# Performance work log

Hardware: AMD Instinct MI355X
Metric: run time of the kernel (lower is better)

The kernel has to match this reference:

```python
import jax, jax.numpy as jnp
import numpy as np

UNITS = 256


def setup_inputs() -> dict:
    key = jax.random.key(0)
    ks = jax.random.split(key, 9)
    B, H, W, C = 8, 64, 64, UNITS
    x = jax.random.normal(ks[0], (B, H, W, C), dtype=jnp.float32)
    # 1x1 Conv2D == per-pixel linear: weight [C_in, C_out], bias [C_out]
    def lin(k):
        return jax.random.normal(k, (C, UNITS), dtype=jnp.float32) * (2.0 / C) ** 0.5
    return {
        "x": x,
        "wq": lin(ks[1]), "bq": jnp.zeros((UNITS,), jnp.float32),
        "wk": lin(ks[2]), "bk": jnp.zeros((UNITS,), jnp.float32),
        "wv": lin(ks[3]), "bv": jnp.zeros((UNITS,), jnp.float32),
        "wp": lin(ks[4]), "bp": jnp.zeros((UNITS,), jnp.float32),
    }


def reference(x, wq, bq, wk, bk, wv, bv, wp, bp):
    B, H, W, C = x.shape
    N = H * W
    scale = jnp.asarray(UNITS, jnp.float32) ** -0.5
    xf = x.reshape(B, N, C)  # 1x1 conv == matmul over channels
    q = xf @ wq + bq
    k = xf @ wk + bk
    v = xf @ wv + bv
    # (b,h,w,c)x(b,H,W,c)->(b,h,w,H,W) flattened to (b,N,N)
    scores = jnp.einsum('bnc,bmc->bnm', q, k) * scale
    attn = jax.nn.softmax(scores, axis=-1)
    out = jnp.einsum('bnm,bmc->bnc', attn, v)
    proj = out @ wp + bp
    return x + proj.reshape(B, H, W, UNITS)
```

## Files before the change

kernel.cpp:

```cpp
#include <hip/hip_runtime.h>


typedef _Float16 half8 __attribute__((ext_vector_type(8)));
typedef _Float16 half4 __attribute__((ext_vector_type(4)));
typedef float f32x4 __attribute__((ext_vector_type(4)));
typedef float f32x16 __attribute__((ext_vector_type(16)));
typedef unsigned int u32x4 __attribute__((ext_vector_type(4)));
typedef unsigned int u32x2 __attribute__((ext_vector_type(2)));

#define MFMA16(a, b, c) __builtin_amdgcn_mfma_f32_16x16x32_f16((a), (b), (c), 0, 0, 0)
#define MFMA32(a, b, c) __builtin_amdgcn_mfma_f32_32x32x16_f16((a), (b), (c), 0, 0, 0)

#if __has_builtin(__builtin_amdgcn_exp2f)
#define EXP2(x) __builtin_amdgcn_exp2f(x)
#else
#define EXP2(x) exp2f(x)
#endif

#define QSCALE 0.09016843898f
#define ESHIFT 11.5415603f

__device__ __forceinline__ void lds_load16(const void* g, void* l) {
    __builtin_amdgcn_global_load_lds(
        (const __attribute__((address_space(1))) unsigned int*)g,
        (__attribute__((address_space(3))) unsigned int*)l, 16, 0, 0);
}

__global__ __launch_bounds__(256)
void wt_prep(const float* __restrict__ w0, const float* __restrict__ w1,
             const float* __restrict__ w2, const float* __restrict__ w3,
             _Float16* __restrict__ outw)
{
    __shared__ _Float16 sT[64 * 72];
    const int z = blockIdx.z;
    const float* W = (z == 0) ? w0 : (z == 1) ? w1 : (z == 2) ? w2 : w3;
    _Float16* O = outw + z * 65536;
    const int kb = blockIdx.x * 64, nb = blockIdx.y * 64;
    const int t = threadIdx.x;
    const int r = t >> 4, c4 = (t & 15) * 4;
#pragma unroll
    for (int i = 0; i < 4; ++i) {
        f32x4 ld = *(const f32x4*)(W + (size_t)(kb + r + i * 16) * 256 + nb + c4);
#pragma unroll
        for (int j = 0; j < 4; ++j) sT[(c4 + j) * 72 + r + i * 16] = (_Float16)ld[j];
    }
    __syncthreads();
#pragma unroll
    for (int i = 0; i < 4; ++i) {
        int n = r + i * 16;
        *(u32x2*)&O[(size_t)(nb + n) * 256 + kb + c4] = *(const u32x2*)&sT[n * 72 + c4];
    }
}

__global__ __launch_bounds__(256)
void qkv_gemm(const float* __restrict__ x, const _Float16* __restrict__ wt,
              const float* __restrict__ bq, const float* __restrict__ bk,
              const float* __restrict__ bv,
              _Float16* __restrict__ qo, _Float16* __restrict__ ko,
              _Float16* __restrict__ vo)
{
    __shared__ _Float16 smem[4 * 2560];
    _Float16* sA = smem;

    const int tid  = threadIdx.x;
    const int w    = tid >> 6;
    const int lane = tid & 63;
    const int quad = lane >> 4;
    const int l16  = lane & 15;
    const int m0   = blockIdx.x * 64;
    const int n0   = blockIdx.y * 64;
    const int rS = tid >> 2, cS = (tid & 3) << 3;

    const float* ap = x + (size_t)(m0 + rS) * 256 + cS;
    f32x4 a0 = *(const f32x4*)ap, a1 = *(const f32x4*)(ap + 4);
    u32x4 bst[3];
#pragma unroll
    for (int o = 0; o < 3; ++o)
        bst[o] = *(const u32x4*)(wt + o * 65536 + (size_t)(n0 + rS) * 256 + cS);

    f32x4 zero4 = {0.f, 0.f, 0.f, 0.f};
    f32x4 acc[3][4];
#pragma unroll
    for (int o = 0; o < 3; ++o)
#pragma unroll
        for (int mt = 0; mt < 4; ++mt) acc[o][mt] = zero4;

    for (int it = 0; it < 8; ++it) {
        __syncthreads();
        half8 t;
#pragma unroll
        for (int j = 0; j < 4; ++j) { t[j] = (_Float16)a0[j]; t[j + 4] = (_Float16)a1[j]; }
        *(half8*)&sA[rS * 40 + cS] = t;
#pragma unroll
        for (int o = 0; o < 3; ++o)
            *(u32x4*)&smem[2560 * (o + 1) + rS * 40 + cS] = bst[o];
        __syncthreads();
        if (it < 7) {
            int k0 = (it + 1) * 32;
            const float* ap2 = x + (size_t)(m0 + rS) * 256 + k0 + cS;
            a0 = *(const f32x4*)ap2; a1 = *(const f32x4*)(ap2 + 4);
#pragma unroll
            for (int o = 0; o < 3; ++o)
                bst[o] = *(const u32x4*)(wt + o * 65536 + (size_t)(n0 + rS) * 256 + k0 + cS);
        }
        half8 af[4];
#pragma unroll
        for (int mt = 0; mt < 4; ++mt)
            af[mt] = *(const half8*)&sA[(mt * 16 + l16) * 40 + quad * 8];
#pragma unroll
        for (int o = 0; o < 3; ++o) {
            half8 bf = *(const half8*)&smem[2560 * (o + 1) + (16 * w + l16) * 40 + quad * 8];
#pragma unroll
            for (int mt = 0; mt < 4; ++mt)
                acc[o][mt] = MFMA16(af[mt], bf, acc[o][mt]);
        }
    }

    const int col = n0 + 16 * w + l16;
#pragma unroll
    for (int mt = 0; mt < 4; ++mt) {
#pragma unroll
        for (int reg = 0; reg < 4; ++reg) {
            int row = m0 + 16 * mt + quad * 4 + reg;
            qo[(size_t)row * 256 + col] = (_Float16)((acc[0][mt][reg] + bq[col]) * QSCALE);
            ko[(size_t)row * 256 + col] = (_Float16)(acc[1][mt][reg] + bk[col]);
        }
    }
    __syncthreads();
    _Float16* sT = smem;
#pragma unroll
    for (int mt = 0; mt < 4; ++mt)
#pragma unroll
        for (int reg = 0; reg < 4; ++reg)
            sT[(16 * w + l16) * 72 + 16 * mt + quad * 4 + reg] =
                (_Float16)(acc[2][mt][reg] + bv[col]);
    __syncthreads();
    int ch = tid >> 2, po = (tid & 3) << 4;
    int bb = m0 >> 12, pix = m0 & 4095;
    _Float16* dst = vo + (size_t)bb * 1048576 + (size_t)(n0 + ch) * 4096 + pix + po;
    *(u32x4*)dst       = *(const u32x4*)&sT[ch * 72 + po];
    *(u32x4*)(dst + 8) = *(const u32x4*)&sT[ch * 72 + po + 8];
}

__global__ __launch_bounds__(256)
void proj_gemm(const _Float16* __restrict__ opart, const float* __restrict__ lpart,
               const _Float16* __restrict__ Wt, const float* __restrict__ bias,
               const float* __restrict__ resid, float* __restrict__ out)
{
    __shared__ _Float16 smem[2 * 2560];
    _Float16* sA = smem;
    _Float16* sB = smem + 2560;

    const int tid  = threadIdx.x;
    const int w    = tid >> 6;
    const int lane = tid & 63;
    const int quad = lane >> 4;
    const int l16  = lane & 15;
    const int m0   = blockIdx.x * 64;
    const int n0   = blockIdx.y * 64;
    const int rS = tid >> 2, cS = (tid & 3) << 3;

    const _Float16* o1p = opart;
    const _Float16* o2p = opart + 8388608;
    const int row = m0 + rS;
    const float inv = 1.0f / (lpart[row] + lpart[32768 + row]);

    u32x4 a1v = *(const u32x4*)(o1p + (size_t)row * 256 + cS);
    u32x4 a2v = *(const u32x4*)(o2p + (size_t)row * 256 + cS);
    u32x4 bst = *(const u32x4*)(Wt + (size_t)(n0 + rS) * 256 + cS);

    f32x4 zero4 = {0.f, 0.f, 0.f, 0.f};
    f32x4 acc[4] = {zero4, zero4, zero4, zero4};

    for (int it = 0; it < 8; ++it) {
        __syncthreads();
        {
            half8 h1 = *(half8*)&a1v, h2 = *(half8*)&a2v, t;
#pragma unroll
            for (int j = 0; j < 8; ++j)
                t[j] = (_Float16)(((float)h1[j] + (float)h2[j]) * inv);
            *(half8*)&sA[rS * 40 + cS] = t;
        }
        *(u32x4*)&sB[rS * 40 + cS] = bst;
        __syncthreads();
        if (it < 7) {
            int k0 = (it + 1) * 32;
            a1v = *(const u32x4*)(o1p + (size_t)row * 256 + k0 + cS);
            a2v = *(const u32x4*)(o2p + (size_t)row * 256 + k0 + cS);
            bst = *(const u32x4*)(Wt + (size_t)(n0 + rS) * 256 + k0 + cS);
        }
        half8 af = *(const half8*)&sA[(16 * w + l16) * 40 + quad * 8];
#pragma unroll
        for (int nt = 0; nt < 4; ++nt) {
            half8 bf = *(const half8*)&sB[(nt * 16 + l16) * 40 + quad * 8];
            acc[nt] = MFMA16(af, bf, acc[nt]);
        }
    }
#pragma unroll
    for (int nt = 0; nt < 4; ++nt) {
#pragma unroll
        for (int reg = 0; reg < 4; ++reg) {
            int orow = m0 + 16 * w + quad * 4 + reg;
            int col = n0 + nt * 16 + l16;
            out[(size_t)orow * 256 + col] =
                acc[nt][reg] + bias[col] + resid[(size_t)orow * 256 + col];
        }
    }
}

__global__ __launch_bounds__(512, 2)
void attn_kernel(const _Float16* __restrict__ q, const _Float16* __restrict__ k,
                 const _Float16* __restrict__ vt, _Float16* __restrict__ opart,
                 float* __restrict__ lpart)
{
    extern __shared__ char smem[];
    char* sKb = smem;
    char* sVb = smem + 32768;

    const int tid  = threadIdx.x;
    const int w    = tid >> 6;
    const int lane = tid & 63;
    const int l31  = lane & 31;
    const int hi   = lane >> 5;
    const int kh   = blockIdx.x & 1;
    const int qg   = (blockIdx.x >> 1) & 15;
    const int b    = blockIdx.x >> 5;

    const _Float16* kb = k  + (size_t)b * 1048576 + (size_t)kh * 524288;
    const _Float16* vb = vt + (size_t)b * 1048576 + kh * 2048;
    const int rowbase = qg * 256 + w * 32;

    half8 qf[16];
    {
        const _Float16* q0 = q + (size_t)(b * 4096 + rowbase + l31) * 256 + hi * 8;
#pragma unroll
        for (int s = 0; s < 16; ++s) qf[s] = *(const half8*)(q0 + s * 16);
    }

    f32x16 o[8];
#pragma unroll
    for (int i = 0; i < 8; ++i)
#pragma unroll
        for (int j = 0; j < 16; ++j) o[i][j] = 0.f;
    float ls = 0.f;

    const int koffL = l31 * 256 + hi * 8;

#pragma unroll
    for (int j = 0; j < 2; ++j) {
        int s = w * 2 + j;
        lds_load16(kb + koffL + s * 16, sKb + s * 1024);
        int ct = s >> 1, ks = s & 1;
        lds_load16(vb + (size_t)(32 * ct + l31) * 4096 + 16 * ks + 8 * hi,
                   sVb + s * 1024);
    }

    for (int kt = 0; kt < 64; ++kt) {
        const int p = kt & 1;
        __syncthreads();

        if (kt < 63) {
            const _Float16* ktb = kb + (size_t)(kt + 1) * 8192;
            const _Float16* vtb = vb + (kt + 1) * 32;
            char* dK = sKb + (1 - p) * 16384;
            char* dV = sVb + (1 - p) * 16384;
#pragma unroll
            for (int j = 0; j < 2; ++j) {
                int s = w * 2 + j;
                lds_load16(ktb + koffL + s * 16, dK + s * 1024);
                int ct = s >> 1, ks = s & 1;
                lds_load16(vtb + (size_t)(32 * ct + l31) * 4096 + 16 * ks + 8 * hi,
                           dV + s * 1024);
            }
        }

        const char* K = sKb + p * 16384;
        const char* V = sVb + p * 16384;

        f32x16 saA, saB;
#pragma unroll
        for (int j = 0; j < 16; ++j) { saA[j] = 0.f; saB[j] = 0.f; }
#pragma unroll
        for (int s = 0; s < 16; s += 2) {
            half8 a0 = *(const half8*)(K + s * 1024 + lane * 16);
            half8 a1 = *(const half8*)(K + (s + 1) * 1024 + lane * 16);
            saA = MFMA32(a0, qf[s], saA);
            saB = MFMA32(a1, qf[s + 1], saB);
        }

#pragma unroll
        for (int j = 0; j < 16; ++j) saA[j] += saB[j];
        unsigned int c[8];
#pragma unroll
        for (int qq = 0; qq < 4; ++qq) {
            float p0 = EXP2(saA[qq * 4 + 0] - ESHIFT);
            float p1 = EXP2(saA[qq * 4 + 1] - ESHIFT);
            float p2 = EXP2(saA[qq * 4 + 2] - ESHIFT);
            float p3 = EXP2(saA[qq * 4 + 3] - ESHIFT);
            ls += (p0 + p1) + (p2 + p3);
            c[2 * qq]     = __builtin_bit_cast(unsigned int,
                                __builtin_amdgcn_cvt_pkrtz(p0, p1));
            c[2 * qq + 1] = __builtin_bit_cast(unsigned int,
                                __builtin_amdgcn_cvt_pkrtz(p2, p3));
        }
        u32x2 s0 = __builtin_amdgcn_permlane32_swap(c[0], c[2], false, false);
        u32x2 s1 = __builtin_amdgcn_permlane32_swap(c[1], c[3], false, false);
        u32x2 s2 = __builtin_amdgcn_permlane32_swap(c[4], c[6], false, false);
        u32x2 s3 = __builtin_amdgcn_permlane32_swap(c[5], c[7], false, false);
        u32x4 w0 = {s0[0], s1[0], s0[1], s1[1]};
        u32x4 w1 = {s2[0], s3[0], s2[1], s3[1]};
        half8 pf0 = __builtin_bit_cast(half8, w0);
        half8 pf1 = __builtin_bit_cast(half8, w1);

#pragma unroll
        for (int ct = 0; ct < 8; ++ct) {
            half8 b0 = *(const half8*)(V + (ct * 2 + 0) * 1024 + lane * 16);
            half8 b1 = *(const half8*)(V + (ct * 2 + 1) * 1024 + lane * 16);
            o[ct] = MFMA32(pf0, b0, o[ct]);
            o[ct] = MFMA32(pf1, b1, o[ct]);
        }
    }

    ls += __shfl_xor(ls, 32);
    _Float16* po = opart + (size_t)kh * 8388608 + (size_t)(b * 4096 + rowbase) * 256;
    float* pl = lpart + kh * 32768 + b * 4096 + rowbase;
    if (hi == 0) pl[l31] = ls;
#pragma unroll
    for (int ct = 0; ct < 8; ++ct) {
#pragma unroll
        for (int reg = 0; reg < 16; ++reg) {
            int row = (reg & 3) + 8 * (reg >> 2) + 4 * hi;
            po[(size_t)row * 256 + ct * 32 + l31] = (_Float16)o[ct][reg];
        }
    }
}

extern "C" void kernel_launch(void* const* d_in, const int* in_sizes, int n_in,
                              void* d_out, int out_size, void* d_ws, size_t ws_size,
                              hipStream_t stream) {
    const float* x  = (const float*)d_in[0];
    const float* wq = (const float*)d_in[1];
    const float* bq = (const float*)d_in[2];
    const float* wk = (const float*)d_in[3];
    const float* bk = (const float*)d_in[4];
    const float* wv = (const float*)d_in[5];
    const float* bv = (const float*)d_in[6];
    const float* wp = (const float*)d_in[7];
    const float* bp = (const float*)d_in[8];

    _Float16* qws  = (_Float16*)d_ws;
    _Float16* kws  = qws + 8388608;
    _Float16* vtws = kws + 8388608;
    _Float16* ows  = vtws + 8388608;
    _Float16* wt   = ows + 16777216;
    float*    lws  = (float*)(wt + 262144);

    dim3 blk(256);

    (void)hipFuncSetAttribute((const void*)attn_kernel,
                              hipFuncAttributeMaxDynamicSharedMemorySize, 65536);

    wt_prep<<<dim3(4, 4, 4), blk, 0, stream>>>(wq, wk, wv, wp, wt);
    qkv_gemm<<<dim3(512, 4), blk, 0, stream>>>(x, wt, bq, bk, bv, qws, kws, vtws);
    attn_kernel<<<dim3(256), dim3(512), 65536, stream>>>(qws, kws, vtws, ows, lws);
    proj_gemm<<<dim3(512, 4), blk, 0, stream>>>(ows, lws, wt + 196608, bp, x, (float*)d_out);
}
```

Before: 291.2 us.

## Stage full-K A tile in LDS once and stream B fragments from registers

```diff
diff --git a/kernel.cpp b/kernel.cpp
--- a/kernel.cpp
+++ b/kernel.cpp
@@ -52,15 +52,14 @@
     }
 }
 
-__global__ __launch_bounds__(256)
+__global__ __launch_bounds__(256, 4)
 void qkv_gemm(const float* __restrict__ x, const _Float16* __restrict__ wt,
               const float* __restrict__ bq, const float* __restrict__ bk,
               const float* __restrict__ bv,
               _Float16* __restrict__ qo, _Float16* __restrict__ ko,
               _Float16* __restrict__ vo)
 {
-    __shared__ _Float16 smem[4 * 2560];
-    _Float16* sA = smem;
+    __shared__ _Float16 sA[16384];
 
     const int tid  = threadIdx.x;
     const int w    = tid >> 6;
@@ -69,14 +68,27 @@
     const int l16  = lane & 15;
     const int m0   = blockIdx.x * 64;
     const int n0   = blockIdx.y * 64;
-    const int rS = tid >> 2, cS = (tid & 3) << 3;
-
-    const float* ap = x + (size_t)(m0 + rS) * 256 + cS;
-    f32x4 a0 = *(const f32x4*)ap, a1 = *(const f32x4*)(ap + 4);
-    u32x4 bst[3];
+    const int rS = tid >> 2, jS = tid & 3;
+
+    {
+        const float* ap = x + (size_t)(m0 + rS) * 256 + jS * 8;
+        const int blk_base = (rS >> 4) * 64 + jS * 16 + (rS & 15);
+#pragma unroll
+        for (int i = 0; i < 8; ++i) {
+            f32x4 a0 = *(const f32x4*)(ap + 32 * i);
+            f32x4 a1 = *(const f32x4*)(ap + 32 * i + 4);
+            half8 t;
+#pragma unroll
+            for (int j = 0; j < 4; ++j) { t[j] = (_Float16)a0[j]; t[j + 4] = (_Float16)a1[j]; }
+            *(half8*)&sA[(i * 256 + blk_base) * 8] = t;
+        }
+    }
+
+    const int nrow = (n0 + 16 * w + l16) * 256 + quad * 8;
+    u32x4 bcur[3];
 #pragma unroll
     for (int o = 0; o < 3; ++o)
-        bst[o] = *(const u32x4*)(wt + o * 65536 + (size_t)(n0 + rS) * 256 + cS);
+        bcur[o] = *(const u32x4*)(wt + o * 65536 + nrow);
 
     f32x4 zero4 = {0.f, 0.f, 0.f, 0.f};
     f32x4 acc[3][4];
@@ -85,35 +97,27 @@
 #pragma unroll
         for (int mt = 0; mt < 4; ++mt) acc[o][mt] = zero4;
 
+    __syncthreads();
+
     for (int it = 0; it < 8; ++it) {
-        __syncthreads();
-        half8 t;
-#pragma unroll
-        for (int j = 0; j < 4; ++j) { t[j] = (_Float16)a0[j]; t[j + 4] = (_Float16)a1[j]; }
-        *(half8*)&sA[rS * 40 + cS] = t;
+        half8 af[4];
+#pragma unroll
+        for (int mt = 0; mt < 4; ++mt)
+            af[mt] = *(const half8*)&sA[((it * 4 + mt) * 64 + quad * 16 + l16) * 8];
+        u32x4 bnext[3];
+        int itn = (it + 1) & 7;
 #pragma unroll
         for (int o = 0; o < 3; ++o)
-            *(u32x4*)&smem[2560 * (o + 1) + rS * 40 + cS] = bst[o];
-        __syncthreads();
-        if (it < 7) {
-            int k0 = (it + 1) * 32;
-            const float* ap2 = x + (size_t)(m0 + rS) * 256 + k0 + cS;
-            a0 = *(const f32x4*)ap2; a1 = *(const f32x4*)(ap2 + 4);
-#pragma unroll
-            for (int o = 0; o < 3; ++o)
-                bst[o] = *(const u32x4*)(wt + o * 65536 + (size_t)(n0 + rS) * 256 + k0 + cS);
-        }
-        half8 af[4];
-#pragma unroll
-        for (int mt = 0; mt < 4; ++mt)
-            af[mt] = *(const half8*)&sA[(mt * 16 + l16) * 40 + quad * 8];
+            bnext[o] = *(const u32x4*)(wt + o * 65536 + nrow + itn * 32);
 #pragma unroll
         for (int o = 0; o < 3; ++o) {
-            half8 bf = *(const half8*)&smem[2560 * (o + 1) + (16 * w + l16) * 40 + quad * 8];
+            half8 bf = __builtin_bit_cast(half8, bcur[o]);
 #pragma unroll
             for (int mt = 0; mt < 4; ++mt)
                 acc[o][mt] = MFMA16(af[mt], bf, acc[o][mt]);
         }
+#pragma unroll
+        for (int o = 0; o < 3; ++o) bcur[o] = bnext[o];
     }
 
     const int col = n0 + 16 * w + l16;
@@ -127,7 +131,7 @@
         }
     }
     __syncthreads();
-    _Float16* sT = smem;
+    _Float16* sT = sA;
 #pragma unroll
     for (int mt = 0; mt < 4; ++mt)
 #pragma unroll
@@ -142,14 +146,12 @@
     *(u32x4*)(dst + 8) = *(const u32x4*)&sT[ch * 72 + po + 8];
 }
 
-__global__ __launch_bounds__(256)
+__global__ __launch_bounds__(256, 4)
 void proj_gemm(const _Float16* __restrict__ opart, const float* __restrict__ lpart,
                const _Float16* __restrict__ Wt, const float* __restrict__ bias,
                const float* __restrict__ resid, float* __restrict__ out)
 {
-    __shared__ _Float16 smem[2 * 2560];
-    _Float16* sA = smem;
-    _Float16* sB = smem + 2560;
+    __shared__ _Float16 sA[16384];
 
     const int tid  = threadIdx.x;
     const int w    = tid >> 6;
@@ -158,43 +160,48 @@
     const int l16  = lane & 15;
     const int m0   = blockIdx.x * 64;
     const int n0   = blockIdx.y * 64;
-    const int rS = tid >> 2, cS = (tid & 3) << 3;
-
-    const _Float16* o1p = opart;
-    const _Float16* o2p = opart + 8388608;
-    const int row = m0 + rS;
-    const float inv = 1.0f / (lpart[row] + lpart[32768 + row]);
-
-    u32x4 a1v = *(const u32x4*)(o1p + (size_t)row * 256 + cS);
-    u32x4 a2v = *(const u32x4*)(o2p + (size_t)row * 256 + cS);
-    u32x4 bst = *(const u32x4*)(Wt + (size_t)(n0 + rS) * 256 + cS);
+    const int rS = tid >> 2, jS = tid & 3;
+
+    {
+        const int row = m0 + rS;
+        const float inv = 1.0f / (lpart[row] + lpart[32768 + row]);
+        const _Float16* o1p = opart + (size_t)row * 256 + jS * 8;
+        const _Float16* o2p = o1p + 8388608;
+        const int blk_base = (rS >> 4) * 64 + jS * 16 + (rS & 15);
+#pragma unroll
+        for (int i = 0; i < 8; ++i) {
+            half8 h1 = *(const half8*)(o1p + 32 * i);
+            half8 h2 = *(const half8*)(o2p + 32 * i);
+            half8 t;
+#pragma unroll
+            for (int j = 0; j < 8; ++j)
+                t[j] = (_Float16)(((float)h1[j] + (float)h2[j]) * inv);
+            *(half8*)&sA[(i * 256 + blk_base) * 8] = t;
+        }
+    }
+
+    u32x4 bcur[4];
+#pragma unroll
+    for (int nt = 0; nt < 4; ++nt)
+        bcur[nt] = *(const u32x4*)(Wt + (n0 + nt * 16 + l16) * 256 + quad * 8);
 
     f32x4 zero4 = {0.f, 0.f, 0.f, 0.f};
     f32x4 acc[4] = {zero4, zero4, zero4, zero4};
 
+    __syncthreads();
+
     for (int it = 0; it < 8; ++it) {
-        __syncthreads();
-        {
-            half8 h1 = *(half8*)&a1v, h2 = *(half8*)&a2v, t;
-#pragma unroll
-            for (int j = 0; j < 8; ++j)
-                t[j] = (_Float16)(((float)h1[j] + (float)h2[j]) * inv);
-            *(half8*)&sA[rS * 40 + cS] = t;
-        }
-        *(u32x4*)&sB[rS * 40 + cS] = bst;
-        __syncthreads();
-        if (it < 7) {
-            int k0 = (it + 1) * 32;
-            a1v = *(const u32x4*)(o1p + (size_t)row * 256 + k0 + cS);
-            a2v = *(const u32x4*)(o2p + (size_t)row * 256 + k0 + cS);
-            bst = *(const u32x4*)(Wt + (size_t)(n0 + rS) * 256 + k0 + cS);
-        }
-        half8 af = *(const half8*)&sA[(16 * w + l16) * 40 + quad * 8];
-#pragma unroll
-        for (int nt = 0; nt < 4; ++nt) {
-            half8 bf = *(const half8*)&sB[(nt * 16 + l16) * 40 + quad * 8];
-            acc[nt] = MFMA16(af, bf, acc[nt]);
-        }
+        half8 af = *(const half8*)&sA[((it * 4 + w) * 64 + quad * 16 + l16) * 8];
+        u32x4 bnext[4];
+        int itn = (it + 1) & 7;
+#pragma unroll
+        for (int nt = 0; nt < 4; ++nt)
+            bnext[nt] = *(const u32x4*)(Wt + (n0 + nt * 16 + l16) * 256 + itn * 32 + quad * 8);
+#pragma unroll
+        for (int nt = 0; nt < 4; ++nt)
+            acc[nt] = MFMA16(af, __builtin_bit_cast(half8, bcur[nt]), acc[nt]);
+#pragma unroll
+        for (int nt = 0; nt < 4; ++nt) bcur[nt] = bnext[nt];
     }
 #pragma unroll
     for (int nt = 0; nt < 4; ++nt) {
```

After: 303.2 us. 4.1% more time.
